# Optimization experiments

Measured on AMD Instinct MI355X. Metric: run time of the kernel, lower is better.

The kernel has to match this reference:

```python
import jax, jax.numpy as jnp
import numpy as np

N = 4096   # num_nodes == nb_items
E = 3      # num_edge types
C = 2      # num_channels
D = 128    # basket_embed_dim
RU = 128   # rnn_units
B = 32     # batch size
L = 20     # max_seq_length
ALPHA = 0.5


def _gtconv(W, A):
    # softmax over edge types, then channel-weighted combine of adjacencies
    f = jax.nn.softmax(W, axis=1)              # [C, E]
    return jnp.einsum('ce,enm->cnm', f, A)     # [C, N, N]


def _normalize(H):
    # remove self loops, then column-degree (in-degree) inverse normalization
    eye = jnp.eye(H.shape[-1], dtype=H.dtype)
    Hn = H * (1.0 - eye)
    deg = Hn.sum(axis=1)                        # scatter_add over col -> [C, N]
    dinv = jnp.where(deg == 0, jnp.zeros_like(deg), 1.0 / deg)
    dinv = jax.lax.stop_gradient(dinv)          # original computes deg under no_grad
    return Hn * dinv[:, None, :]


def _lstm(x, h0, c0, W_ih, W_hh, b_ih, b_hh):
    # single-layer batch-first LSTM, torch gate order (i, f, g, o)
    def step(carry, xt):
        h, c = carry
        z = xt @ W_ih.T + b_ih + h @ W_hh.T + b_hh
        i, f, g, o = jnp.split(z, 4, axis=-1)
        c = jax.nn.sigmoid(f) * c + jax.nn.sigmoid(i) * jnp.tanh(g)
        h = jax.nn.sigmoid(o) * jnp.tanh(c)
        return (h, c), h
    _, ys = jax.lax.scan(step, (h0, c0), jnp.swapaxes(x, 0, 1))
    return jnp.swapaxes(ys, 0, 1)               # [B, L, RU]


def setup_inputs():
    key = jax.random.key(0)
    k = jax.random.split(key, 12)
    A = jax.random.uniform(k[0], (E, N, N), jnp.float32) * (2.0 / N)
    seqs = (jax.random.uniform(k[1], (B, L, N)) < 0.02).astype(jnp.float32)
    seq_len = jax.random.randint(k[2], (B,), 1, L + 1)
    h0 = jnp.zeros((B, RU), jnp.float32)
    c0 = jnp.zeros((B, RU), jnp.float32)
    W1a = 1.0 + 0.1 * jax.random.normal(k[3], (C, E), jnp.float32)
    W1b = 1.0 + 0.1 * jax.random.normal(k[4], (C, E), jnp.float32)
    W2 = 1.0 + 0.1 * jax.random.normal(k[5], (C, E), jnp.float32)
    I_B = jnp.ones((N,), jnp.float32) / N
    lin_w = jax.random.normal(k[6], (C, D, N), jnp.float32) / np.sqrt(N).astype(np.float32)
    lin_b = jnp.zeros((C, D), jnp.float32)
    proj_w = jax.random.normal(k[7], (D, C * D), jnp.float32) / np.sqrt(C * D).astype(np.float32)
    proj_b = jnp.zeros((D,), jnp.float32)
    W_ih = jax.random.normal(k[8], (4 * RU, D), jnp.float32) / np.sqrt(D).astype(np.float32)
    W_hh = jax.random.normal(k[9], (4 * RU, RU), jnp.float32) / np.sqrt(RU).astype(np.float32)
    b_ih = jnp.zeros((4 * RU,), jnp.float32)
    b_hh = jnp.zeros((4 * RU,), jnp.float32)
    h2item_w = jax.random.normal(k[10], (N, RU), jnp.float32) / np.sqrt(RU).astype(np.float32)
    return dict(A=A, seqs=seqs, seq_len=seq_len, h0=h0, c0=c0, W1a=W1a, W1b=W1b,
                W2=W2, I_B=I_B, lin_w=lin_w, lin_b=lin_b, proj_w=proj_w, proj_b=proj_b,
                W_ih=W_ih, W_hh=W_hh, b_ih=b_ih, b_hh=b_hh, h2item_w=h2item_w)


def reference(A, seqs, seq_len, h0, c0, W1a, W1b, W2, I_B, lin_w, lin_b,
              proj_w, proj_b, W_ih, W_hh, b_ih, b_hh, h2item_w):
    # layer 0 (first=True): H[c] = conv1(A)[c] @ conv2(A)[c]  (spspmm, dense form)
    H = jnp.einsum('cij,cjk->cik', _gtconv(W1a, A), _gtconv(W1b, A))
    # layer 1: H[c] = norm(H)[c] @ conv(A)[c]
    H = jnp.einsum('cij,cjk->cik', _normalize(H), _gtconv(W2, A))

    x = seqs.reshape(-1, N)                     # [B*L, nb_items]
    v = jax.nn.relu(I_B)                        # diag(I_B) after relu
    enc = []
    for i in range(C):
        xh = jax.nn.relu(x @ H[i])
        if i == 0:
            e = jax.nn.relu(x * v) + xh         # note: channel-0 formula differs
        else:
            e = jax.nn.relu(x * v + xh)
        enc.append(e @ lin_w[i].T + lin_b[i])
    enc = jnp.concatenate(enc, axis=1)          # [B*L, C*D]
    baskets = (enc @ proj_w.T + proj_b).reshape(B, L, D)

    lstm_out = _lstm(baskets, h0, c0, W_ih, W_hh, b_ih, b_hh)
    idx = jnp.arange(B) * L + (seq_len - 1)
    last = lstm_out.reshape(-1, RU)[idx]        # [B, RU]
    probs = jax.nn.sigmoid(last @ h2item_w.T)   # [B, nb_items]
    return (1.0 - ALPHA) * probs + ALPHA * (probs * v)
```

## Files before the change

### kernel.cpp

```cpp
#include <hip/hip_runtime.h>


typedef float  f4v  __attribute__((ext_vector_type(4)));
typedef short  s8v  __attribute__((ext_vector_type(8)));
typedef unsigned short u16;
typedef unsigned int u32;
typedef u32    u2v  __attribute__((ext_vector_type(2)));
typedef u32    u4v  __attribute__((ext_vector_type(4)));

#define NN 4096
#define MM 640

__device__ __forceinline__ u16 f2bf(float f){
  unsigned int u = __float_as_uint(f);
  u += 0x7FFFu + ((u>>16)&1u);
  return (u16)(u>>16);
}
__device__ __forceinline__ float bf2f(u16 h){ return __uint_as_float(((unsigned int)h)<<16); }
__device__ __forceinline__ float sigm(float x){ return 1.f/(1.f+__expf(-x)); }

__device__ __forceinline__ u32 pkbf(float lo, float hi){
  u32 r;
  asm("v_cvt_pk_bf16_f32 %0, %1, %2" : "=v"(r) : "v"(lo), "v"(hi));
  return r;
}

__device__ __forceinline__ void gload16(const void* g, void* l){
  __builtin_amdgcn_global_load_lds((const __attribute__((address_space(1))) unsigned int*)g,
                                   (__attribute__((address_space(3))) unsigned int*)l, 16, 0, 0);
}

__device__ __forceinline__ void softmax23(const float* __restrict__ W, float f[2][3]){
  #pragma unroll
  for (int c=0;c<2;c++){
    float a=W[c*3+0], b=W[c*3+1], d=W[c*3+2];
    float m=fmaxf(a,fmaxf(b,d));
    float ea=__expf(a-m), eb=__expf(b-m), ed=__expf(d-m);
    float s=1.f/(ea+eb+ed);
    f[c][0]=ea*s; f[c][1]=eb*s; f[c][2]=ed*s;
  }
}

__global__ __launch_bounds__(256)
void k_combine_all(const float* __restrict__ A, const float* __restrict__ W1a,
                   const float* __restrict__ W1b, const float* __restrict__ W2,
                   u16* __restrict__ C1, u16* __restrict__ C2t,
                   u16* __restrict__ C3t, float* __restrict__ r)
{
  __shared__ u16 t2[64][72];
  __shared__ u16 t3[64][72];
  __shared__ float rs[2][64];
  const int tid = threadIdx.x, lane = tid&63;
  const int n0 = blockIdx.x*64, m0 = blockIdx.y*64;
  float fa[2][3], fb[2][3], fc[2][3];
  softmax23(W1a, fa); softmax23(W1b, fb); softmax23(W2, fc);
  if (tid < 128) rs[tid>>6][tid&63] = 0.f;
  const int mb = tid>>4, nb = tid&15;
  f4v a0[4], a1[4], a2[4];
  #pragma unroll
  for (int j=0;j<4;j++){
    const float* ap = A + (size_t)(m0+mb*4+j)*NN + n0 + nb*4;
    a0[j] = *(const f4v*)ap;
    a1[j] = *(const f4v*)(ap + (size_t)NN*NN);
    a2[j] = *(const f4v*)(ap + 2*(size_t)NN*NN);
  }
  #pragma unroll
  for (int c=0;c<2;c++){
    float rp[4] = {};
    #pragma unroll
    for (int j=0;j<4;j++){
      f4v v1 = fa[c][0]*a0[j] + fa[c][1]*a1[j] + fa[c][2]*a2[j];
      u2v o = { pkbf(v1[0],v1[1]), pkbf(v1[2],v1[3]) };
      *(u2v*)(C1 + ((size_t)c*NN + m0+mb*4+j)*NN + n0 + nb*4) = o;
      #pragma unroll
      for (int k=0;k<4;k++) rp[k] += v1[k];
    }
    #pragma unroll
    for (int jj=0;jj<4;jj++){
      f4v c2v, c3v;
      #pragma unroll
      for (int j=0;j<4;j++){
        c2v[j] = fb[c][0]*a0[j][jj] + fb[c][1]*a1[j][jj] + fb[c][2]*a2[j][jj];
        c3v[j] = fc[c][0]*a0[j][jj] + fc[c][1]*a1[j][jj] + fc[c][2]*a2[j][jj];
      }
      *(u2v*)&t2[nb*4+jj][mb*4] = (u2v){ pkbf(c2v[0],c2v[1]), pkbf(c2v[2],c2v[3]) };
      *(u2v*)&t3[nb*4+jj][mb*4] = (u2v){ pkbf(c3v[0],c3v[1]), pkbf(c3v[2],c3v[3]) };
    }
    __syncthreads();
    #pragma unroll
    for (int rep=0;rep<2;rep++){
      const int rw = rep*32 + (tid>>3), l8 = tid&7;
      *(u4v*)(C2t + ((size_t)c*NN + n0+rw)*NN + m0 + l8*8) = *(const u4v*)&t2[rw][l8*8];
      *(u4v*)(C3t + ((size_t)c*NN + n0+rw)*NN + m0 + l8*8) = *(const u4v*)&t3[rw][l8*8];
    }
    #pragma unroll
    for (int k=0;k<4;k++){
      float v = rp[k];
      v += __shfl_xor(v,16); v += __shfl_xor(v,32);
      if (lane < 16) atomicAdd(&rs[c][nb*4+k], v);
    }
    __syncthreads();
  }
  if (tid < 128) atomicAdd(&r[(size_t)(tid>>6)*NN + n0 + (tid&63)], rs[tid>>6][tid&63]);
}

__global__ __launch_bounds__(256)
void k_sparse_y(const float* __restrict__ seqs, const u16* __restrict__ C1,
                u16* __restrict__ y)
{
  __shared__ int idxl[512];
  __shared__ int cnt;
  const int tid = threadIdx.x, row = blockIdx.x;
  if (tid==0) cnt = 0;
  __syncthreads();
  const float* xr = seqs + (size_t)row*NN;
  #pragma unroll
  for (int it=0; it<4; ++it){
    f4v v = *(const f4v*)(xr + it*1024 + tid*4);
    #pragma unroll
    for (int k=0;k<4;k++) if (v[k] > 0.5f){ int p = atomicAdd(&cnt,1); if (p<512) idxl[p] = it*1024+tid*4+k; }
  }
  __syncthreads();
  const int nz = cnt < 512 ? cnt : 512;
  float acc0[16], acc1[16];
  #pragma unroll
  for (int k=0;k<16;k++){ acc0[k]=0.f; acc1[k]=0.f; }
  const int cb = tid*16;
  s8v ca, cb8, cc8, cd8;
  if (nz > 0){
    const u16* r0 = C1 + (size_t)idxl[0]*NN + cb;
    const u16* r1 = r0 + (size_t)NN*NN;
    ca=*(const s8v*)r0; cb8=*(const s8v*)(r0+8); cc8=*(const s8v*)r1; cd8=*(const s8v*)(r1+8);
  }
  for (int p=0;p<nz;++p){
    const int pn = (p+1<nz)? p+1 : p;
    const u16* r0 = C1 + (size_t)idxl[pn]*NN + cb;
    const u16* r1 = r0 + (size_t)NN*NN;
    s8v na=*(const s8v*)r0, nb=*(const s8v*)(r0+8), nc=*(const s8v*)r1, nd=*(const s8v*)(r1+8);
    #pragma unroll
    for (int k=0;k<8;k++){
      acc0[k]   += bf2f((u16)ca[k]);
      acc0[8+k] += bf2f((u16)cb8[k]);
      acc1[k]   += bf2f((u16)cc8[k]);
      acc1[8+k] += bf2f((u16)cd8[k]);
    }
    ca=na; cb8=nb; cc8=nc; cd8=nd;
  }
  u4v o0, o1;
  #pragma unroll
  for (int k=0;k<4;k++){
    o0[k] = pkbf(acc0[2*k], acc0[2*k+1]);
    o1[k] = pkbf(acc0[8+2*k], acc0[9+2*k]);
  }
  u16* y0 = y + (size_t)row*NN + cb;
  *(u4v*)y0 = o0; *(u4v*)(y0+8) = o1;
  #pragma unroll
  for (int k=0;k<4;k++){
    o0[k] = pkbf(acc1[2*k], acc1[2*k+1]);
    o1[k] = pkbf(acc1[8+2*k], acc1[9+2*k]);
  }
  u16* y1 = y0 + (size_t)MM*NN;
  *(u4v*)y1 = o0; *(u4v*)(y1+8) = o1;
}

__global__ __launch_bounds__(256)
void k_diagdeg(const u16* __restrict__ C1, const u16* __restrict__ C2t,
               const float* __restrict__ r, float* __restrict__ diag1,
               float* __restrict__ dinv)
{
  const int tid = threadIdx.x, lane = tid&63;
  const int gw = blockIdx.x*4 + (tid>>6);
  const int c = gw>>12, k = gw&4095;
  const u16* p1 = C1  + ((size_t)c*NN + k)*NN;
  const u16* p2 = C2t + ((size_t)c*NN + k)*NN;
  const float* pr = r + (size_t)c*NN;
  float dd = 0.f, dg = 0.f;
  for (int it=0; it<8; ++it){
    const int j = it*512 + lane*8;
    s8v v1 = *(const s8v*)(p1+j);
    s8v v2 = *(const s8v*)(p2+j);
    f4v r0 = *(const f4v*)(pr+j);
    f4v r1 = *(const f4v*)(pr+j+4);
    #pragma unroll
    for (int q=0;q<8;q++){
      float c2 = bf2f((u16)v2[q]);
      dd += bf2f((u16)v1[q]) * c2;
      dg += ((q<4)? r0[q] : r1[q-4]) * c2;
    }
  }
  #pragma unroll
  for (int m=1;m<64;m<<=1){ dd += __shfl_xor(dd, m); dg += __shfl_xor(dg, m); }
  if (lane==0){
    float deg = dg - dd;
    diag1[(size_t)c*NN+k] = dd;
    dinv[(size_t)c*NN+k]  = (deg==0.f) ? 0.f : 1.f/deg;
  }
}

__global__ __launch_bounds__(256)
void k_gemm_sk(const u16* __restrict__ Xb, const u16* __restrict__ Bt,
               float* __restrict__ part)
{
  __shared__ u16 As[2][128*32];
  __shared__ u16 Bs[2][128*32];
  const int tid = threadIdx.x, lane = tid&63, w = tid>>6;
  const int g = blockIdx.x;
  const int xcd = g & 7, q = g >> 3;
  const int m = q % 5, p = q / 5;
  const int nh = p & 3, ks = (p>>2)&3, c = (p>>4)&1;
  const int m0 = m*128, n0 = (nh*8 + xcd)*128, kb = ks*1024;
  const u16* Ab = Xb + (size_t)c*MM*NN;
  const u16* Bb = Bt + (size_t)c*NN*NN;
  const int srow = lane>>2;
  const int scol = ((lane&3) ^ (srow&3))*8;
  const int fr = lane&15, c0 = lane>>4;
  const int wm = (w>>1)*64, wn = (w&1)*64;
  f4v acc[4][4] = {};
  auto STAGE = [&](int buf, int k0){
    #pragma unroll
    for (int i=0;i<2;i++){
      const int rb = i*64 + w*16;
      gload16(Ab + (size_t)(m0 + rb + srow)*NN + k0 + scol, (void*)&As[buf][rb*32]);
      gload16(Bb + (size_t)(n0 + rb + srow)*NN + k0 + scol, (void*)&Bs[buf][rb*32]);
    }
  };
  STAGE(0, kb);
  __syncthreads();
  int cur = 0;
  for (int k0=0;k0<1024;k0+=32){
    if (k0+32 < 1024) STAGE(cur^1, kb+k0+32);
    s8v a[4], b[4];
    #pragma unroll
    for (int t=0;t<4;t++){
      const int ra = wm + t*16 + fr;
      a[t] = *(const s8v*)&As[cur][ra*32 + ((c0 ^ (ra&3))*8)];
      const int rb2 = wn + t*16 + fr;
      b[t] = *(const s8v*)&Bs[cur][rb2*32 + ((c0 ^ (rb2&3))*8)];
    }
    #pragma unroll
    for (int i=0;i<4;i++)
      #pragma unroll
      for (int j=0;j<4;j++)
        acc[i][j] = __builtin_amdgcn_mfma_f32_16x16x32_bf16(a[i], b[j], acc[i][j], 0, 0, 0);
    __syncthreads();
    cur ^= 1;
  }
  float* pb = part + (size_t)(c*4+ks)*MM*NN;
  #pragma unroll
  for (int i=0;i<4;i++){
    #pragma unroll
    for (int j=0;j<4;j++){
      const int col = n0 + wn + j*16 + fr;
      #pragma unroll
      for (int rr=0;rr<4;rr++){
        const int row = m0 + wm + i*16 + (lane>>4)*4 + rr;
        pb[(size_t)row*NN + col] = acc[i][j][rr];
      }
    }
  }
}

template<int M>
__global__ __launch_bounds__(256)
void k_epi(const float* __restrict__ part, const float* __restrict__ seqs,
           const float* __restrict__ diag1, const float* __restrict__ dinv,
           const float* __restrict__ IB, u16* __restrict__ outp)
{
  const int g = blockIdx.x*256 + threadIdx.x;
  const int c = blockIdx.y;
  const int row = g>>10, col = (g&1023)*4;
  const size_t base = (size_t)row*NN + col;
  f4v z = {0.f,0.f,0.f,0.f};
  #pragma unroll
  for (int ks=0;ks<4;ks++)
    z += *(const f4v*)(part + (size_t)(c*4+ks)*MM*NN + base);
  f4v val;
  if constexpr(M==1){
    f4v x  = *(const f4v*)(seqs + base);
    f4v d  = *(const f4v*)(diag1 + (size_t)c*NN + col);
    f4v dv = *(const f4v*)(dinv  + (size_t)c*NN + col);
    val = (z - x*d) * dv;
  } else {
    f4v x  = *(const f4v*)(seqs + base);
    f4v ib = *(const f4v*)(IB + col);
    #pragma unroll
    for (int k=0;k<4;k++){
      float xh = fmaxf(z[k], 0.f);
      float vv = fmaxf(ib[k], 0.f);
      val[k] = (c==0) ? (fmaxf(x[k]*vv,0.f) + xh) : fmaxf(x[k]*vv + xh, 0.f);
    }
  }
  u2v o = { pkbf(val[0],val[1]), pkbf(val[2],val[3]) };
  *(u2v*)(outp + (size_t)c*MM*NN + base) = o;
}

__global__ __launch_bounds__(256)
void k_cvt(const float* __restrict__ linw, const float* __restrict__ whh,
           u16* __restrict__ linwb, u16* __restrict__ whhb)
{
  const int g = blockIdx.x*256 + threadIdx.x;
  const int i = g*4;
  const int NL = 2*128*NN;
  f4v v; u16* dst;
  if (i < NL){ v = *(const f4v*)(linw + i); dst = linwb + i; }
  else       { v = *(const f4v*)(whh + (i-NL)); dst = whhb + (i-NL); }
  u2v o = { pkbf(v[0],v[1]), pkbf(v[2],v[3]) };
  *(u2v*)dst = o;
}

__global__ __launch_bounds__(256)
void k_lin(const u16* __restrict__ e, const u16* __restrict__ linwb,
           float* __restrict__ encr)
{
  __shared__ u16 As[64*32];
  __shared__ u16 Bs[64*32];
  const int tid=threadIdx.x, lane=tid&63, w=tid>>6;
  const int m0 = blockIdx.x*64, d0 = blockIdx.y*64;
  const int c = blockIdx.z>>4, ks = blockIdx.z&15;
  const u16* Ab = e + (size_t)c*MM*NN;
  const u16* Bb = linwb + (size_t)c*128*NN;
  const int srow=lane>>2, skof=(lane&3)*8, fr=lane&15, fk=(lane>>4)*8;
  const int wm=(w>>1)*32, wn=(w&1)*32;
  f4v acc[2][2];
  #pragma unroll
  for (int i=0;i<2;i++)
    #pragma unroll
    for (int j=0;j<2;j++) acc[i][j] = (f4v){0.f,0.f,0.f,0.f};
  for (int ki=0;ki<8;++ki){
    const int k0 = ks*256 + ki*32;
    gload16(Ab + (size_t)(m0 + w*16 + srow)*NN + k0 + skof, (void*)&As[(w*16)*32]);
    gload16(Bb + (size_t)(d0 + w*16 + srow)*NN + k0 + skof, (void*)&Bs[(w*16)*32]);
    __syncthreads();
    s8v a[2], b[2];
    #pragma unroll
    for (int t=0;t<2;t++) a[t] = *(const s8v*)&As[(wm+t*16+fr)*32+fk];
    #pragma unroll
    for (int t=0;t<2;t++) b[t] = *(const s8v*)&Bs[(wn+t*16+fr)*32+fk];
    #pragma unroll
    for (int i=0;i<2;i++)
      #pragma unroll
      for (int j=0;j<2;j++)
        acc[i][j] = __builtin_amdgcn_mfma_f32_16x16x32_bf16(a[i], b[j], acc[i][j], 0, 0, 0);
    __syncthreads();
  }
  #pragma unroll
  for (int i=0;i<2;i++)
    #pragma unroll
    for (int j=0;j<2;j++){
      const int col = d0 + wn + j*16 + fr;
      #pragma unroll
      for (int rr=0;rr<4;rr++){
        const int row = m0 + wm + i*16 + (lane>>4)*4 + rr;
        atomicAdd(&encr[(size_t)row*256 + c*128 + col], acc[i][j][rr]);
      }
    }
}

__global__ __launch_bounds__(256)
void k_proj(const float* __restrict__ encr, const float* __restrict__ linb,
            const float* __restrict__ pw, const float* __restrict__ pb,
            float* __restrict__ bask)
{
  const int g = blockIdx.x*256 + threadIdx.x;
  const int row = g>>7, d = g&127;
  const float* er = encr + (size_t)row*256;
  const float* wr = pw + (size_t)d*256;
  float acc = pb[d];
  for (int j=0;j<256;j+=4){
    f4v e4 = *(const f4v*)(er+j);
    f4v l4 = *(const f4v*)(linb+j);
    f4v w4 = *(const f4v*)(wr+j);
    acc += (e4[0]+l4[0])*w4[0] + (e4[1]+l4[1])*w4[1] + (e4[2]+l4[2])*w4[2] + (e4[3]+l4[3])*w4[3];
  }
  bask[g] = acc;
}

__global__ __launch_bounds__(256)
void k_xhat(const float* __restrict__ bask, const float* __restrict__ wih,
            const float* __restrict__ bih, const float* __restrict__ bhh,
            float* __restrict__ xh)
{
  const int g = blockIdx.x*256 + threadIdx.x;
  const int row = g>>9, n = g&511;
  const float* br = bask + (size_t)row*128;
  const float* wr = wih + (size_t)n*128;
  float acc = bih[n] + bhh[n];
  for (int k=0;k<128;k+=4){
    f4v b4=*(const f4v*)(br+k); f4v w4=*(const f4v*)(wr+k);
    acc += b4[0]*w4[0]+b4[1]*w4[1]+b4[2]*w4[2]+b4[3]*w4[3];
  }
  const int b = row/20, t = row%20;
  xh[((size_t)t*32 + b)*512 + n] = acc;
}

__global__ __launch_bounds__(512)
void k_lstm(const float* __restrict__ xhat, const u16* __restrict__ whhb,
            const float* __restrict__ h0, const float* __restrict__ c0,
            const int* __restrict__ slen, float* __restrict__ last)
{
  __shared__ float zb[32][512];
  __shared__ float cbuf[32][128];
  __shared__ u16 hb[32][136];
  const int tid = threadIdx.x, lane = tid&63, w = tid>>6;
  for (int i=tid; i<4096; i+=512){ int b=i>>7,u=i&127; cbuf[b][u]=c0[i]; hb[b][u]=f2bf(h0[i]); }
  const int fr = lane&15, fko = (lane>>4)*8;
  s8v bfr[4][4];
  #pragma unroll
  for (int nt=0;nt<4;nt++)
    #pragma unroll
    for (int kf=0;kf<4;kf++)
      bfr[nt][kf] = *(const s8v*)(whhb + (size_t)(w*64 + nt*16 + fr)*128 + kf*32 + fko);
  __syncthreads();
  for (int t=0;t<20;++t){
    s8v af[2][4];
    #pragma unroll
    for (int mt=0;mt<2;mt++)
      #pragma unroll
      for (int kf=0;kf<4;kf++)
        af[mt][kf] = *(const s8v*)&hb[mt*16+fr][kf*32+fko];
    f4v z[2][4];
    #pragma unroll
    for (int mt=0;mt<2;mt++)
      #pragma unroll
      for (int nt=0;nt<4;nt++){
        const int nn2 = w*64 + nt*16 + fr;
        #pragma unroll
        for (int rr=0;rr<4;rr++){
          const int bb = mt*16 + (lane>>4)*4 + rr;
          z[mt][nt][rr] = xhat[((size_t)t*32 + bb)*512 + nn2];
        }
      }
    #pragma unroll
    for (int kf=0;kf<4;kf++)
      #pragma unroll
      for (int mt=0;mt<2;mt++)
        #pragma unroll
        for (int nt=0;nt<4;nt++)
          z[mt][nt] = __builtin_amdgcn_mfma_f32_16x16x32_bf16(af[mt][kf], bfr[nt][kf], z[mt][nt], 0, 0, 0);
    #pragma unroll
    for (int mt=0;mt<2;mt++)
      #pragma unroll
      for (int nt=0;nt<4;nt++){
        const int nn2 = w*64 + nt*16 + fr;
        #pragma unroll
        for (int rr=0;rr<4;rr++){
          const int bb = mt*16 + (lane>>4)*4 + rr;
          zb[bb][nn2] = z[mt][nt][rr];
        }
      }
    __syncthreads();
    for (int p=tid; p<4096; p+=512){
      const int b=p>>7, u=p&127;
      float zi=zb[b][u], zf=zb[b][128+u], zg=zb[b][256+u], zo=zb[b][384+u];
      float ii=sigm(zi), ff=sigm(zf), gg=tanhf(zg), oo=sigm(zo);
      float cn = ff*cbuf[b][u] + ii*gg;
      float hn = oo*tanhf(cn);
      cbuf[b][u]=cn; hb[b][u]=f2bf(hn);
      if (t == slen[b]-1) last[p] = hn;
    }
    __syncthreads();
  }
}

__global__ __launch_bounds__(256)
void k_final(const float* __restrict__ last, const float* __restrict__ h2w,
             const float* __restrict__ IB, float* __restrict__ out)
{
  __shared__ float ls[128];
  const int b = blockIdx.y;
  const int n = blockIdx.x*256 + threadIdx.x;
  if (threadIdx.x < 128) ls[threadIdx.x] = last[b*128 + threadIdx.x];
  __syncthreads();
  const float* wr = h2w + (size_t)n*128;
  float acc = 0.f;
  for (int k=0;k<128;k+=4){
    f4v w4 = *(const f4v*)(wr+k);
    acc += w4[0]*ls[k] + w4[1]*ls[k+1] + w4[2]*ls[k+2] + w4[3]*ls[k+3];
  }
  const float vn = fmaxf(IB[n], 0.f);
  out[(size_t)b*NN + n] = (0.5f + 0.5f*vn) * sigm(acc);
}

extern "C" void kernel_launch(void* const* d_in, const int* in_sizes, int n_in,
                              void* d_out, int out_size, void* d_ws, size_t ws_size,
                              hipStream_t stream)
{
  const float* A    = (const float*)d_in[0];
  const float* seqs = (const float*)d_in[1];
  const int*   slen = (const int*)  d_in[2];
  const float* h0   = (const float*)d_in[3];
  const float* c0   = (const float*)d_in[4];
  const float* W1a  = (const float*)d_in[5];
  const float* W1b  = (const float*)d_in[6];
  const float* W2   = (const float*)d_in[7];
  const float* IB   = (const float*)d_in[8];
  const float* linw = (const float*)d_in[9];
  const float* linb = (const float*)d_in[10];
  const float* pw   = (const float*)d_in[11];
  const float* pb   = (const float*)d_in[12];
  const float* wih  = (const float*)d_in[13];
  const float* whh  = (const float*)d_in[14];
  const float* bih  = (const float*)d_in[15];
  const float* bhh  = (const float*)d_in[16];
  const float* h2w  = (const float*)d_in[17];
  (void)in_sizes; (void)n_in; (void)out_size; (void)ws_size;

  char* ws = (char*)d_ws;
  size_t off = 0;
  auto alloc = [&](size_t sz)->void*{ void* p = ws + off; off += (sz + 255) & ~(size_t)255; return p; };
  u16*   C1    = (u16*)  alloc((size_t)2*NN*NN*2);
  u16*   C2t   = (u16*)  alloc((size_t)2*NN*NN*2);
  u16*   C3t   = (u16*)  alloc((size_t)2*NN*NN*2);
  u16*   y     = (u16*)  alloc((size_t)2*MM*NN*2);
  u16*   u     = (u16*)  alloc((size_t)2*MM*NN*2);
  float* part  = (float*)alloc((size_t)4*2*MM*NN*4);
  float* r     = (float*)alloc((size_t)2*NN*4);
  float* diag1 = (float*)alloc((size_t)2*NN*4);
  float* dinv  = (float*)alloc((size_t)2*NN*4);
  u16*   linwb = (u16*)  alloc((size_t)2*128*NN*2);
  u16*   whhb  = (u16*)  alloc((size_t)512*128*2);
  float* encr  = (float*)alloc((size_t)MM*256*4);
  float* bask  = (float*)alloc((size_t)MM*128*4);
  float* xh    = (float*)alloc((size_t)20*32*512*4);
  float* last  = (float*)alloc((size_t)32*128*4);

  hipMemsetAsync(r, 0, (size_t)2*NN*4, stream);
  hipMemsetAsync(encr, 0, (size_t)MM*256*4, stream);

  k_combine_all<<<dim3(64,64),256,0,stream>>>(A, W1a, W1b, W2, C1, C2t, C3t, r);
  k_sparse_y<<<MM,256,0,stream>>>(seqs, C1, y);
  k_diagdeg<<<2048,256,0,stream>>>(C1, C2t, r, diag1, dinv);
  k_gemm_sk<<<1280,256,0,stream>>>(y, C2t, part);
  k_epi<1><<<dim3(2560,2),256,0,stream>>>(part, seqs, diag1, dinv, IB, u);
  k_gemm_sk<<<1280,256,0,stream>>>(u, C3t, part);
  u16* e = y;
  k_epi<2><<<dim3(2560,2),256,0,stream>>>(part, seqs, diag1, dinv, IB, e);
  k_cvt<<<1088,256,0,stream>>>(linw, whh, linwb, whhb);
  k_lin<<<dim3(10,2,32),256,0,stream>>>(e, linwb, encr);
  k_proj<<<320,256,0,stream>>>(encr, linb, pw, pb, bask);
  k_xhat<<<1280,256,0,stream>>>(bask, wih, bih, bhh, xh);
  k_lstm<<<1,512,0,stream>>>(xh, whhb, h0, c0, slen, last);
  k_final<<<dim3(16,32),256,0,stream>>>(last, h2w, IB, (float*)d_out);
}
```

Before: 533.5 us.

## Split sparse row gather across column halves and pipeline GEMM loads with vmcnt waits

The sparse-row accumulation kernel now launches two blocks per row, each covering half the columns with 8 elements per thread. It keeps two gathered rows in flight to raise memory-level parallelism and occupancy. The split-K GEMM replaces its __syncthreads with explicit s_waitcnt vmcnt plus raw s_barrier, so the next stage's global-to-LDS loads stay outstanding while the current tile is consumed. This relies on the exact per-thread count of outstanding loads being 4, which is fragile if the compiler reorders or changes the load count.

```diff
diff --git a/kernel.cpp b/kernel.cpp
--- a/kernel.cpp
+++ b/kernel.cpp
@@ -122,45 +122,48 @@
   }
   __syncthreads();
   const int nz = cnt < 512 ? cnt : 512;
-  float acc0[16], acc1[16];
-  #pragma unroll
-  for (int k=0;k<16;k++){ acc0[k]=0.f; acc1[k]=0.f; }
-  const int cb = tid*16;
-  s8v ca, cb8, cc8, cd8;
+  float acc0[8], acc1[8];
+  #pragma unroll
+  for (int k=0;k<8;k++){ acc0[k]=0.f; acc1[k]=0.f; }
+  const int cb = blockIdx.y*2048 + tid*8;
+  s8v a0, c0, a1, c1;
   if (nz > 0){
     const u16* r0 = C1 + (size_t)idxl[0]*NN + cb;
-    const u16* r1 = r0 + (size_t)NN*NN;
-    ca=*(const s8v*)r0; cb8=*(const s8v*)(r0+8); cc8=*(const s8v*)r1; cd8=*(const s8v*)(r1+8);
-  }
-  for (int p=0;p<nz;++p){
-    const int pn = (p+1<nz)? p+1 : p;
-    const u16* r0 = C1 + (size_t)idxl[pn]*NN + cb;
-    const u16* r1 = r0 + (size_t)NN*NN;
-    s8v na=*(const s8v*)r0, nb=*(const s8v*)(r0+8), nc=*(const s8v*)r1, nd=*(const s8v*)(r1+8);
-    #pragma unroll
-    for (int k=0;k<8;k++){
-      acc0[k]   += bf2f((u16)ca[k]);
-      acc0[8+k] += bf2f((u16)cb8[k]);
-      acc1[k]   += bf2f((u16)cc8[k]);
-      acc1[8+k] += bf2f((u16)cd8[k]);
-    }
-    ca=na; cb8=nb; cc8=nc; cd8=nd;
+    a0 = *(const s8v*)r0; c0 = *(const s8v*)(r0 + (size_t)NN*NN);
+  }
+  if (nz > 1){
+    const u16* r1 = C1 + (size_t)idxl[1]*NN + cb;
+    a1 = *(const s8v*)r1; c1 = *(const s8v*)(r1 + (size_t)NN*NN);
+  }
+  int p = 0;
+  for (; p+1 < nz; p += 2){
+    s8v ta = a0, tc = c0;
+    if (p+2 < nz){
+      const u16* rn = C1 + (size_t)idxl[p+2]*NN + cb;
+      a0 = *(const s8v*)rn; c0 = *(const s8v*)(rn + (size_t)NN*NN);
+    }
+    #pragma unroll
+    for (int k=0;k<8;k++){ acc0[k] += bf2f((u16)ta[k]); acc1[k] += bf2f((u16)tc[k]); }
+    s8v ua = a1, uc = c1;
+    if (p+3 < nz){
+      const u16* rn = C1 + (size_t)idxl[p+3]*NN + cb;
+      a1 = *(const s8v*)rn; c1 = *(const s8v*)(rn + (size_t)NN*NN);
+    }
+    #pragma unroll
+    for (int k=0;k<8;k++){ acc0[k] += bf2f((u16)ua[k]); acc1[k] += bf2f((u16)uc[k]); }
+  }
+  if (p < nz){
+    #pragma unroll
+    for (int k=0;k<8;k++){ acc0[k] += bf2f((u16)a0[k]); acc1[k] += bf2f((u16)c0[k]); }
   }
   u4v o0, o1;
   #pragma unroll
   for (int k=0;k<4;k++){
     o0[k] = pkbf(acc0[2*k], acc0[2*k+1]);
-    o1[k] = pkbf(acc0[8+2*k], acc0[9+2*k]);
-  }
-  u16* y0 = y + (size_t)row*NN + cb;
-  *(u4v*)y0 = o0; *(u4v*)(y0+8) = o1;
-  #pragma unroll
-  for (int k=0;k<4;k++){
-    o0[k] = pkbf(acc1[2*k], acc1[2*k+1]);
-    o1[k] = pkbf(acc1[8+2*k], acc1[9+2*k]);
-  }
-  u16* y1 = y0 + (size_t)MM*NN;
-  *(u4v*)y1 = o0; *(u4v*)(y1+8) = o1;
+    o1[k] = pkbf(acc1[2*k], acc1[2*k+1]);
+  }
+  *(u4v*)(y + (size_t)row*NN + cb) = o0;
+  *(u4v*)(y + (size_t)MM*NN + (size_t)row*NN + cb) = o1;
 }
 
 __global__ __launch_bounds__(256)
@@ -225,10 +228,16 @@
     }
   };
   STAGE(0, kb);
-  __syncthreads();
   int cur = 0;
   for (int k0=0;k0<1024;k0+=32){
-    if (k0+32 < 1024) STAGE(cur^1, kb+k0+32);
+    if (k0+32 < 1024){
+      STAGE(cur^1, kb+k0+32);
+      asm volatile("s_waitcnt vmcnt(4)" ::: "memory");
+    } else {
+      asm volatile("s_waitcnt vmcnt(0)" ::: "memory");
+    }
+    __builtin_amdgcn_s_barrier();
+    __builtin_amdgcn_sched_barrier(0);
     s8v a[4], b[4];
     #pragma unroll
     for (int t=0;t<4;t++){
@@ -242,7 +251,8 @@
       #pragma unroll
       for (int j=0;j<4;j++)
         acc[i][j] = __builtin_amdgcn_mfma_f32_16x16x32_bf16(a[i], b[j], acc[i][j], 0, 0, 0);
-    __syncthreads();
+    asm volatile("" ::: "memory");
+    __builtin_amdgcn_s_barrier();
     cur ^= 1;
   }
   float* pb = part + (size_t)(c*4+ks)*MM*NN;
@@ -528,7 +538,7 @@
   hipMemsetAsync(encr, 0, (size_t)MM*256*4, stream);
 
   k_combine_all<<<dim3(64,64),256,0,stream>>>(A, W1a, W1b, W2, C1, C2t, C3t, r);
-  k_sparse_y<<<MM,256,0,stream>>>(seqs, C1, y);
+  k_sparse_y<<<dim3(MM,2),256,0,stream>>>(seqs, C1, y);
   k_diagdeg<<<2048,256,0,stream>>>(C1, C2t, r, diag1, dinv);
   k_gemm_sk<<<1280,256,0,stream>>>(y, C2t, part);
   k_epi<1><<<dim3(2560,2),256,0,stream>>>(part, seqs, diag1, dinv, IB, u);
```

Measured after the change: 563.7 us. 5.7% more time.
